# Performance work log

Measured on AMD Instinct MI355X. Metric: run time of the kernel, lower is better.

Reference implementation:

```python
import jax, jax.numpy as jnp
import numpy as np

N_EMB = 1024
N_HEAD = 16
HEAD_DIM = N_EMB // N_HEAD


def setup_inputs() -> dict:
    key = jax.random.key(0)
    k_x, k_wa, k_ba, k_wp, k_bp = jax.random.split(key, 5)
    B, S = 4, 2048
    scale = 1.0 / np.sqrt(N_EMB)
    return {
        "x": jax.random.normal(k_x, (B, S, N_EMB), dtype=jnp.float32),
        "W_attn": jax.random.normal(k_wa, (N_EMB, 3 * N_EMB), dtype=jnp.float32) * scale,
        "b_attn": jax.random.normal(k_ba, (3 * N_EMB,), dtype=jnp.float32) * 0.01,
        "W_proj": jax.random.normal(k_wp, (N_EMB, N_EMB), dtype=jnp.float32) * scale,
        "b_proj": jax.random.normal(k_bp, (N_EMB,), dtype=jnp.float32) * 0.01,
    }


def _attention(x, W_attn, b_attn, W_proj, b_proj):
    B, S, E = x.shape
    qkv = x @ W_attn + b_attn  # [B, S, 3E]
    q, k, v = jnp.split(qkv, 3, axis=-1)
    # [B, H, S, D]
    q = q.reshape(B, S, N_HEAD, HEAD_DIM).transpose(0, 2, 1, 3)
    k = k.reshape(B, S, N_HEAD, HEAD_DIM).transpose(0, 2, 1, 3)
    v = v.reshape(B, S, N_HEAD, HEAD_DIM).transpose(0, 2, 1, 3)
    scores = jnp.einsum("bhqd,bhkd->bhqk", q, k) / jnp.sqrt(jnp.asarray(HEAD_DIM, x.dtype))
    causal = jnp.tril(jnp.ones((S, S), dtype=bool))
    scores = jnp.where(causal, scores, jnp.asarray(-jnp.inf, x.dtype))
    probs = jax.nn.softmax(scores, axis=-1)
    y = jnp.einsum("bhqk,bhkd->bhqd", probs, v)  # [B, H, S, D]
    y = y.transpose(0, 2, 1, 3).reshape(B, S, E)
    return y @ W_proj + b_proj


def reference(x, W_attn, b_attn, W_proj, b_proj):
    return _attention(x, W_attn, b_attn, W_proj, b_proj)
```

## Files before the change

### kernel.cpp

```cpp
#include <hip/hip_runtime.h>
#include <hip/hip_bf16.h>

typedef __bf16 bf16x8 __attribute__((ext_vector_type(8)));
typedef __bf16 bf16x4 __attribute__((ext_vector_type(4)));
typedef float f32x4 __attribute__((ext_vector_type(4)));

#define MFMA16(a, b, c) __builtin_amdgcn_mfma_f32_16x16x32_bf16(a, b, c, 0, 0, 0)

#define BATCH 4
#define SEQ   2048
#define EMB   1024
#define NHEAD 16
#define HDIM  64
#define ROWS  (BATCH * SEQ)
#define N_QKV (3 * EMB)
#define BH_STRIDE (SEQ * HDIM)

__device__ __forceinline__ void gload_lds16(const __bf16* gp, __bf16* lp) {
  __builtin_amdgcn_global_load_lds(
      (const __attribute__((address_space(1))) void*)gp,
      (__attribute__((address_space(3))) void*)lp, 16, 0, 0);
}

__global__ void cast_f32_to_bf16_x4(const float* __restrict__ src,
                                    __bf16* __restrict__ dst, int n4) {
  int i = blockIdx.x * blockDim.x + threadIdx.x;
  if (i >= n4) return;
  float4 f = ((const float4*)src)[i];
  bf16x4 o;
  o.x = (__bf16)f.x; o.y = (__bf16)f.y; o.z = (__bf16)f.z; o.w = (__bf16)f.w;
  ((bf16x4*)dst)[i] = o;
}

__global__ void transpose_to_bf16(const float* __restrict__ src,
                                  __bf16* __restrict__ dst, int R, int C) {
  __shared__ float t[32][33];
  int c0 = blockIdx.x * 32, r0 = blockIdx.y * 32;
  int tx = threadIdx.x, ty = threadIdx.y;
#pragma unroll
  for (int i = 0; i < 32; i += 8)
    t[ty + i][tx] = src[(size_t)(r0 + ty + i) * C + c0 + tx];
  __syncthreads();
#pragma unroll
  for (int i = 0; i < 32; i += 8)
    dst[(size_t)(c0 + ty + i) * R + r0 + tx] = (__bf16)t[tx][ty + i];
}

__global__ __launch_bounds__(256) void gemm_qkv(
    const __bf16* __restrict__ A, const __bf16* __restrict__ Bt,
    const float* __restrict__ bias,
    __bf16* __restrict__ Qt, __bf16* __restrict__ Kt, __bf16* __restrict__ Vt) {
  const int K = EMB;
  __shared__ __align__(16) __bf16 sA[128 * 32];
  __shared__ __align__(16) __bf16 sB[128 * 32];
  int id = blockIdx.x;
  int xcd = id & 7, j5 = id >> 3;
  int by = j5 >> 3;
  int bx = xcd * 8 + (j5 & 7);
  int m0 = by * 128, n0 = bx * 128;
  int tid = threadIdx.x;
  int wave = tid >> 6, lane = tid & 63;
  int wr = wave >> 1, wc = wave & 1;
  int l16 = lane & 15, quad = lane >> 4, quad4 = quad * 4;
  int f1 = tid * 8;
  int r1 = f1 >> 5, c1 = f1 & 31;
  int f2 = f1 + 2048;
  int r2 = f2 >> 5, c2 = f2 & 31;
  f32x4 acc[4][4] = {};
  for (int k0 = 0; k0 < K; k0 += 32) {
    gload_lds16(A + (size_t)(m0 + r1) * K + k0 + c1, &sA[wave * 512]);
    gload_lds16(A + (size_t)(m0 + r2) * K + k0 + c2, &sA[2048 + wave * 512]);
    gload_lds16(Bt + (size_t)(n0 + r1) * K + k0 + c1, &sB[wave * 512]);
    gload_lds16(Bt + (size_t)(n0 + r2) * K + k0 + c2, &sB[2048 + wave * 512]);
    __syncthreads();
    bf16x8 a[4], b[4];
#pragma unroll
    for (int i = 0; i < 4; i++)
      a[i] = *(const bf16x8*)(sA + (wr * 64 + i * 16 + l16) * 32 + quad * 8);
#pragma unroll
    for (int j = 0; j < 4; j++)
      b[j] = *(const bf16x8*)(sB + (wc * 64 + j * 16 + l16) * 32 + quad * 8);
#pragma unroll
    for (int i = 0; i < 4; i++)
#pragma unroll
      for (int j = 0; j < 4; j++) acc[i][j] = MFMA16(a[i], b[j], acc[i][j]);
    __syncthreads();
  }
  const float KSC = 0.18033688011112043f;
  int sec = m0 >> 10;
#pragma unroll
  for (int i = 0; i < 4; i++) {
    int e0 = m0 + wr * 64 + i * 16 + quad4;
    float4 bv4 = *(const float4*)(bias + e0);
    int h = (e0 & 1023) >> 6, d0 = e0 & 63;
#pragma unroll
    for (int j = 0; j < 4; j++) {
      int scol = n0 + wc * 64 + j * 16 + l16;
      int bidx = scol >> 11, s = scol & 2047;
      size_t base = (size_t)(bidx * NHEAD + h) * BH_STRIDE;
      float v0 = acc[i][j][0] + bv4.x;
      float v1 = acc[i][j][1] + bv4.y;
      float v2 = acc[i][j][2] + bv4.z;
      float v3 = acc[i][j][3] + bv4.w;
      if (sec == 0) {
        int idx = (s >> 4) * 1024 + (d0 >> 5) * 512 + ((d0 >> 3) & 3) * 128 +
                  (s & 15) * 8 + (d0 & 7);
        bf16x4 o4;
        o4.x = (__bf16)(v0 * KSC); o4.y = (__bf16)(v1 * KSC);
        o4.z = (__bf16)(v2 * KSC); o4.w = (__bf16)(v3 * KSC);
        *(bf16x4*)(Qt + base + idx) = o4;
      } else if (sec == 1) {
        int idx = (s >> 6) * 4096 + ((s >> 4) & 3) * 1024 + (d0 >> 5) * 512 +
                  ((d0 >> 3) & 3) * 128 + (s & 15) * 8 + (d0 & 7);
        bf16x4 o4;
        o4.x = (__bf16)v0; o4.y = (__bf16)v1;
        o4.z = (__bf16)v2; o4.w = (__bf16)v3;
        *(bf16x4*)(Kt + base + idx) = o4;
      } else {
        int idx = (s >> 6) * 4096 + (d0 >> 4) * 1024 + ((s >> 5) & 1) * 512 +
                  ((s >> 3) & 3) * 128 + (s & 7) + quad4 * 8;
        Vt[base + idx] = (__bf16)v0;
        Vt[base + idx + 8] = (__bf16)v1;
        Vt[base + idx + 16] = (__bf16)v2;
        Vt[base + idx + 24] = (__bf16)v3;
      }
    }
  }
}

#define PS2 68
__global__ __launch_bounds__(256, 3) void attn_fwd(
    const __bf16* __restrict__ Qt, const __bf16* __restrict__ Kt,
    const __bf16* __restrict__ Vt, __bf16* __restrict__ Y) {
  __shared__ __align__(16) __bf16 sK[2][4096];
  __shared__ __align__(16) __bf16 sV[2][4096];
  __shared__ __align__(16) __bf16 pbuf[4][32 * PS2];
  int id = blockIdx.x;
  int g = id >> 6;
  int qb = 15 - g;
  int hb = id & 63;
  int h = hb >> 2, b = hb & 3;
  int tid = threadIdx.x;
  int wave = tid >> 6, lane = tid & 63;
  int l16 = lane & 15, quad = lane >> 4, quad4 = quad * 4;
  int q0 = qb * 128;
  size_t bh = (size_t)b * NHEAD + h;
  const __bf16* Qh = Qt + bh * BH_STRIDE;
  const __bf16* Kh = Kt + bh * BH_STRIDE;
  const __bf16* Vh = Vt + bh * BH_STRIDE;
  int mq = q0 + wave * 32;
  const __bf16* qbase = Qh + (size_t)(mq >> 4) * 1024 + lane * 8;
  bf16x8 qa0 = *(const bf16x8*)(qbase);
  bf16x8 qa1 = *(const bf16x8*)(qbase + 512);
  bf16x8 qb0 = *(const bf16x8*)(qbase + 1024);
  bf16x8 qb1 = *(const bf16x8*)(qbase + 1536);
  f32x4 accA[4] = {}, accB[4] = {};
  float lA = 0.f, lB = 0.f;
  const float NEG_INF = -__builtin_inff();
  __bf16* pwA = pbuf[wave];
  __bf16* pwB = pbuf[wave] + 16 * PS2;
  int nt = (q0 + 128) >> 6;
  gload_lds16(Kh + tid * 8, sK[0] + tid * 8);
  gload_lds16(Kh + 2048 + tid * 8, sK[0] + 2048 + tid * 8);
  gload_lds16(Vh + tid * 8, sV[0] + tid * 8);
  gload_lds16(Vh + 2048 + tid * 8, sV[0] + 2048 + tid * 8);
  __syncthreads();
  int cur = 0;
  for (int it = 0; it < nt; ++it) {
    int kt = it * 64;
    if (it + 1 < nt) {
      const __bf16* kg = Kh + (size_t)(it + 1) * 4096 + tid * 8;
      const __bf16* vg = Vh + (size_t)(it + 1) * 4096 + tid * 8;
      __bf16* dK = sK[cur ^ 1] + tid * 8;
      __bf16* dV = sV[cur ^ 1] + tid * 8;
      gload_lds16(kg, dK);
      gload_lds16(kg + 2048, dK + 2048);
      gload_lds16(vg, dV);
      gload_lds16(vg + 2048, dV + 2048);
    }
    const __bf16* sKc = sK[cur];
    const __bf16* sVc = sV[cur];
    bool diag = (kt + 64 > mq);
    int relA = mq + l16 - kt;
#pragma unroll
    for (int t = 0; t < 4; t++) {
      bf16x8 ka = *(const bf16x8*)(sKc + t * 1024 + lane * 8);
      bf16x8 kb = *(const bf16x8*)(sKc + t * 1024 + 512 + lane * 8);
      f32x4 zA = {}, zB = {};
      zA = MFMA16(ka, qa0, zA);
      zA = MFMA16(kb, qa1, zA);
      zB = MFMA16(ka, qb0, zB);
      zB = MFMA16(kb, qb1, zB);
      int kl = t * 16 + quad4;
      float pA[4], pB[4];
      if (diag) {
        int relB = relA + 16;
#pragma unroll
        for (int r = 0; r < 4; r++) {
          pA[r] = __builtin_amdgcn_exp2f(kl + r > relA ? NEG_INF : zA[r]);
          pB[r] = __builtin_amdgcn_exp2f(kl + r > relB ? NEG_INF : zB[r]);
        }
      } else {
#pragma unroll
        for (int r = 0; r < 4; r++) {
          pA[r] = __builtin_amdgcn_exp2f(zA[r]);
          pB[r] = __builtin_amdgcn_exp2f(zB[r]);
        }
      }
      lA += (pA[0] + pA[1]) + (pA[2] + pA[3]);
      lB += (pB[0] + pB[1]) + (pB[2] + pB[3]);
      bf16x4 oA, oB;
      oA.x = (__bf16)pA[0]; oA.y = (__bf16)pA[1];
      oA.z = (__bf16)pA[2]; oA.w = (__bf16)pA[3];
      oB.x = (__bf16)pB[0]; oB.y = (__bf16)pB[1];
      oB.z = (__bf16)pB[2]; oB.w = (__bf16)pB[3];
      *(bf16x4*)(pwA + l16 * PS2 + kl) = oA;
      *(bf16x4*)(pwB + l16 * PS2 + kl) = oB;
    }
    bf16x8 pA0 = *(const bf16x8*)(pwA + l16 * PS2 + quad * 8);
    bf16x8 pA1 = *(const bf16x8*)(pwA + l16 * PS2 + 32 + quad * 8);
    bf16x8 pB0 = *(const bf16x8*)(pwB + l16 * PS2 + quad * 8);
    bf16x8 pB1 = *(const bf16x8*)(pwB + l16 * PS2 + 32 + quad * 8);
#pragma unroll
    for (int jj = 0; jj < 4; jj++) {
      bf16x8 va = *(const bf16x8*)(sVc + jj * 1024 + lane * 8);
      bf16x8 vb = *(const bf16x8*)(sVc + jj * 1024 + 512 + lane * 8);
      accA[jj] = MFMA16(va, pA0, accA[jj]);
      accA[jj] = MFMA16(vb, pA1, accA[jj]);
      accB[jj] = MFMA16(va, pB0, accB[jj]);
      accB[jj] = MFMA16(vb, pB1, accB[jj]);
    }
    __syncthreads();
    cur ^= 1;
  }
  lA += __shfl_xor(lA, 16); lA += __shfl_xor(lA, 32);
  lB += __shfl_xor(lB, 16); lB += __shfl_xor(lB, 32);
  float invA = 1.f / lA, invB = 1.f / lB;
  int gqA = mq + l16, gqB = mq + 16 + l16;
#pragma unroll
  for (int jj = 0; jj < 4; jj++) {
    bf16x4 oA, oB;
    oA.x = (__bf16)(accA[jj][0] * invA);
    oA.y = (__bf16)(accA[jj][1] * invA);
    oA.z = (__bf16)(accA[jj][2] * invA);
    oA.w = (__bf16)(accA[jj][3] * invA);
    oB.x = (__bf16)(accB[jj][0] * invB);
    oB.y = (__bf16)(accB[jj][1] * invB);
    oB.z = (__bf16)(accB[jj][2] * invB);
    oB.w = (__bf16)(accB[jj][3] * invB);
    *(bf16x4*)(Y + ((size_t)b * SEQ + gqA) * EMB + h * HDIM + jj * 16 + quad4) = oA;
    *(bf16x4*)(Y + ((size_t)b * SEQ + gqB) * EMB + h * HDIM + jj * 16 + quad4) = oB;
  }
}

__global__ __launch_bounds__(256) void gemm_proj(
    const __bf16* __restrict__ A, const __bf16* __restrict__ Bt,
    const float* __restrict__ bias, float* __restrict__ out) {
  const int K = EMB;
  __shared__ __align__(16) __bf16 sA[128 * 32];
  __shared__ __align__(16) __bf16 sB[128 * 32];
  int id = blockIdx.x;
  int lid = (id & 7) * (512 >> 3) + (id >> 3);
  int bx = lid & 7, by = lid >> 3;
  int m0 = by * 128, n0 = bx * 128;
  int tid = threadIdx.x;
  int wave = tid >> 6, lane = tid & 63;
  int wr = wave >> 1, wc = wave & 1;
  int l16 = lane & 15, quad = lane >> 4;
  int f1 = tid * 8;
  int r1 = f1 >> 5, c1 = f1 & 31;
  int f2 = f1 + 2048;
  int r2 = f2 >> 5, c2 = f2 & 31;
  f32x4 acc[4][4] = {};
  for (int k0 = 0; k0 < K; k0 += 32) {
    gload_lds16(A + (size_t)(m0 + r1) * K + k0 + c1, &sA[wave * 512]);
    gload_lds16(A + (size_t)(m0 + r2) * K + k0 + c2, &sA[2048 + wave * 512]);
    gload_lds16(Bt + (size_t)(n0 + r1) * K + k0 + c1, &sB[wave * 512]);
    gload_lds16(Bt + (size_t)(n0 + r2) * K + k0 + c2, &sB[2048 + wave * 512]);
    __syncthreads();
    bf16x8 a[4], b[4];
#pragma unroll
    for (int i = 0; i < 4; i++)
      a[i] = *(const bf16x8*)(sA + (wr * 64 + i * 16 + l16) * 32 + quad * 8);
#pragma unroll
    for (int j = 0; j < 4; j++)
      b[j] = *(const bf16x8*)(sB + (wc * 64 + j * 16 + l16) * 32 + quad * 8);
#pragma unroll
    for (int i = 0; i < 4; i++)
#pragma unroll
      for (int j = 0; j < 4; j++) acc[i][j] = MFMA16(a[i], b[j], acc[i][j]);
    __syncthreads();
  }
#pragma unroll
  for (int i = 0; i < 4; i++) {
    int row = m0 + wr * 64 + i * 16 + quad * 4;
#pragma unroll
    for (int j = 0; j < 4; j++) {
      int col = n0 + wc * 64 + j * 16 + l16;
      float bv = bias[col];
#pragma unroll
      for (int r = 0; r < 4; r++)
        out[(size_t)(row + r) * EMB + col] = acc[i][j][r] + bv;
    }
  }
}

extern "C" void kernel_launch(void* const* d_in, const int* in_sizes, int n_in,
                              void* d_out, int out_size, void* d_ws, size_t ws_size,
                              hipStream_t stream) {
  const float* x      = (const float*)d_in[0];
  const float* W_attn = (const float*)d_in[1];
  const float* b_attn = (const float*)d_in[2];
  const float* W_proj = (const float*)d_in[3];
  const float* b_proj = (const float*)d_in[4];
  float* out = (float*)d_out;

  char* ws = (char*)d_ws;
  size_t off = 0;
  __bf16* xb   = (__bf16*)(ws + off); off += (size_t)ROWS * EMB * 2;
  __bf16* Wa_t = (__bf16*)(ws + off); off += (size_t)N_QKV * EMB * 2;
  __bf16* Wp_t = (__bf16*)(ws + off); off += (size_t)EMB * EMB * 2;
  __bf16* Qt   = (__bf16*)(ws + off); off += (size_t)ROWS * EMB * 2;
  __bf16* Kt   = (__bf16*)(ws + off); off += (size_t)ROWS * EMB * 2;
  __bf16* Vt   = (__bf16*)(ws + off); off += (size_t)ROWS * EMB * 2;
  __bf16* Yb   = (__bf16*)(ws + off); off += (size_t)ROWS * EMB * 2;

  {
    int n4 = ROWS * EMB / 4;
    cast_f32_to_bf16_x4<<<(n4 + 255) / 256, 256, 0, stream>>>(x, xb, n4);
    dim3 blk(32, 8);
    transpose_to_bf16<<<dim3(N_QKV / 32, EMB / 32), blk, 0, stream>>>(W_attn, Wa_t, EMB, N_QKV);
    transpose_to_bf16<<<dim3(EMB / 32, EMB / 32), blk, 0, stream>>>(W_proj, Wp_t, EMB, EMB);
  }
  gemm_qkv<<<dim3(1536), 256, 0, stream>>>(Wa_t, xb, b_attn, Qt, Kt, Vt);
  attn_fwd<<<dim3((SEQ / 128) * NHEAD * BATCH), 256, 0, stream>>>(Qt, Kt, Vt, Yb);
  gemm_proj<<<dim3(512), 256, 0, stream>>>(Yb, Wp_t, b_proj, out);
}
```

Measured before the change: 253.6 us.

## Keep softmax probabilities in registers by permuting V layout, skip masked tiles

The V tensor layout written by the QKV projection is permuted so the MFMA output fragment of the score tile can be fed directly as the B operand of the PV MFMA. This removes the per-wave LDS round trip for probabilities, along with its buffer and the extra LDS traffic. The change also skips compute for key tiles that lie fully above the causal diagonal for a wave, raises wave priority around the MFMA section, and increases the launch-bounds occupancy hint from 3 to 4 blocks. Correctness depends on the new V index mapping exactly matching the register k-ordering, and the higher occupancy hint may force register spills.

```diff
diff --git a/kernel.cpp b/kernel.cpp
--- a/kernel.cpp
+++ b/kernel.cpp
@@ -118,7 +118,8 @@
         *(bf16x4*)(Kt + base + idx) = o4;
       } else {
         int idx = (s >> 6) * 4096 + (d0 >> 4) * 1024 + ((s >> 5) & 1) * 512 +
-                  ((s >> 3) & 3) * 128 + (s & 7) + quad4 * 8;
+                  ((s >> 2) & 3) * 128 + ((s >> 4) & 1) * 4 + (s & 3) +
+                  quad4 * 8;
         Vt[base + idx] = (__bf16)v0;
         Vt[base + idx + 8] = (__bf16)v1;
         Vt[base + idx + 16] = (__bf16)v2;
@@ -128,13 +129,11 @@
   }
 }
 
-#define PS2 68
-__global__ __launch_bounds__(256, 3) void attn_fwd(
+__global__ __launch_bounds__(256, 4) void attn_fwd(
     const __bf16* __restrict__ Qt, const __bf16* __restrict__ Kt,
     const __bf16* __restrict__ Vt, __bf16* __restrict__ Y) {
   __shared__ __align__(16) __bf16 sK[2][4096];
   __shared__ __align__(16) __bf16 sV[2][4096];
-  __shared__ __align__(16) __bf16 pbuf[4][32 * PS2];
   int id = blockIdx.x;
   int g = id >> 6;
   int qb = 15 - g;
@@ -157,8 +156,6 @@
   f32x4 accA[4] = {}, accB[4] = {};
   float lA = 0.f, lB = 0.f;
   const float NEG_INF = -__builtin_inff();
-  __bf16* pwA = pbuf[wave];
-  __bf16* pwB = pbuf[wave] + 16 * PS2;
   int nt = (q0 + 128) >> 6;
   gload_lds16(Kh + tid * 8, sK[0] + tid * 8);
   gload_lds16(Kh + 2048 + tid * 8, sK[0] + 2048 + tid * 8);
@@ -178,57 +175,72 @@
       gload_lds16(vg, dV);
       gload_lds16(vg + 2048, dV + 2048);
     }
-    const __bf16* sKc = sK[cur];
-    const __bf16* sVc = sV[cur];
-    bool diag = (kt + 64 > mq);
-    int relA = mq + l16 - kt;
-#pragma unroll
-    for (int t = 0; t < 4; t++) {
-      bf16x8 ka = *(const bf16x8*)(sKc + t * 1024 + lane * 8);
-      bf16x8 kb = *(const bf16x8*)(sKc + t * 1024 + 512 + lane * 8);
-      f32x4 zA = {}, zB = {};
-      zA = MFMA16(ka, qa0, zA);
-      zA = MFMA16(kb, qa1, zA);
-      zB = MFMA16(ka, qb0, zB);
-      zB = MFMA16(kb, qb1, zB);
-      int kl = t * 16 + quad4;
-      float pA[4], pB[4];
-      if (diag) {
-        int relB = relA + 16;
-#pragma unroll
-        for (int r = 0; r < 4; r++) {
-          pA[r] = __builtin_amdgcn_exp2f(kl + r > relA ? NEG_INF : zA[r]);
-          pB[r] = __builtin_amdgcn_exp2f(kl + r > relB ? NEG_INF : zB[r]);
+    if (kt <= mq + 31) {
+      const __bf16* sKc = sK[cur];
+      const __bf16* sVc = sV[cur];
+      bool diag = (kt + 64 > mq);
+      int relA = mq + l16 - kt;
+      int relB = relA + 16;
+      bf16x8 PA0, PA1, PB0, PB1;
+      __builtin_amdgcn_s_setprio(1);
+#pragma unroll
+      for (int t = 0; t < 4; t++) {
+        bf16x8 ka = *(const bf16x8*)(sKc + t * 1024 + lane * 8);
+        bf16x8 kb = *(const bf16x8*)(sKc + t * 1024 + 512 + lane * 8);
+        f32x4 zA = {}, zB = {};
+        zA = MFMA16(ka, qa0, zA);
+        zA = MFMA16(kb, qa1, zA);
+        zB = MFMA16(ka, qb0, zB);
+        zB = MFMA16(kb, qb1, zB);
+        int kl = t * 16 + quad4;
+        float pA[4], pB[4];
+        if (diag) {
+#pragma unroll
+          for (int r = 0; r < 4; r++) {
+            pA[r] = __builtin_amdgcn_exp2f(kl + r > relA ? NEG_INF : zA[r]);
+            pB[r] = __builtin_amdgcn_exp2f(kl + r > relB ? NEG_INF : zB[r]);
+          }
+        } else {
+#pragma unroll
+          for (int r = 0; r < 4; r++) {
+            pA[r] = __builtin_amdgcn_exp2f(zA[r]);
+            pB[r] = __builtin_amdgcn_exp2f(zB[r]);
+          }
         }
-      } else {
-#pragma unroll
-        for (int r = 0; r < 4; r++) {
-          pA[r] = __builtin_amdgcn_exp2f(zA[r]);
-          pB[r] = __builtin_amdgcn_exp2f(zB[r]);
+        lA += (pA[0] + pA[1]) + (pA[2] + pA[3]);
+        lB += (pB[0] + pB[1]) + (pB[2] + pB[3]);
+        if (t == 0) {
+          PA0[0] = (__bf16)pA[0]; PA0[1] = (__bf16)pA[1];
+          PA0[2] = (__bf16)pA[2]; PA0[3] = (__bf16)pA[3];
+          PB0[0] = (__bf16)pB[0]; PB0[1] = (__bf16)pB[1];
+          PB0[2] = (__bf16)pB[2]; PB0[3] = (__bf16)pB[3];
+        } else if (t == 1) {
+          PA0[4] = (__bf16)pA[0]; PA0[5] = (__bf16)pA[1];
+          PA0[6] = (__bf16)pA[2]; PA0[7] = (__bf16)pA[3];
+          PB0[4] = (__bf16)pB[0]; PB0[5] = (__bf16)pB[1];
+          PB0[6] = (__bf16)pB[2]; PB0[7] = (__bf16)pB[3];
+        } else if (t == 2) {
+          PA1[0] = (__bf16)pA[0]; PA1[1] = (__bf16)pA[1];
+          PA1[2] = (__bf16)pA[2]; PA1[3] = (__bf16)pA[3];
+          PB1[0] = (__bf16)pB[0]; PB1[1] = (__bf16)pB[1];
+          PB1[2] = (__bf16)pB[2]; PB1[3] = (__bf16)pB[3];
+        } else {
+          PA1[4] = (__bf16)pA[0]; PA1[5] = (__bf16)pA[1];
+          PA1[6] = (__bf16)pA[2]; PA1[7] = (__bf16)pA[3];
+          PB1[4] = (__bf16)pB[0]; PB1[5] = (__bf16)pB[1];
+          PB1[6] = (__bf16)pB[2]; PB1[7] = (__bf16)pB[3];
         }
       }
-      lA += (pA[0] + pA[1]) + (pA[2] + pA[3]);
-      lB += (pB[0] + pB[1]) + (pB[2] + pB[3]);
-      bf16x4 oA, oB;
-      oA.x = (__bf16)pA[0]; oA.y = (__bf16)pA[1];
-      oA.z = (__bf16)pA[2]; oA.w = (__bf16)pA[3];
-      oB.x = (__bf16)pB[0]; oB.y = (__bf16)pB[1];
-      oB.z = (__bf16)pB[2]; oB.w = (__bf16)pB[3];
-      *(bf16x4*)(pwA + l16 * PS2 + kl) = oA;
-      *(bf16x4*)(pwB + l16 * PS2 + kl) = oB;
-    }
-    bf16x8 pA0 = *(const bf16x8*)(pwA + l16 * PS2 + quad * 8);
-    bf16x8 pA1 = *(const bf16x8*)(pwA + l16 * PS2 + 32 + quad * 8);
-    bf16x8 pB0 = *(const bf16x8*)(pwB + l16 * PS2 + quad * 8);
-    bf16x8 pB1 = *(const bf16x8*)(pwB + l16 * PS2 + 32 + quad * 8);
-#pragma unroll
-    for (int jj = 0; jj < 4; jj++) {
-      bf16x8 va = *(const bf16x8*)(sVc + jj * 1024 + lane * 8);
-      bf16x8 vb = *(const bf16x8*)(sVc + jj * 1024 + 512 + lane * 8);
-      accA[jj] = MFMA16(va, pA0, accA[jj]);
-      accA[jj] = MFMA16(vb, pA1, accA[jj]);
-      accB[jj] = MFMA16(va, pB0, accB[jj]);
-      accB[jj] = MFMA16(vb, pB1, accB[jj]);
+#pragma unroll
+      for (int jj = 0; jj < 4; jj++) {
+        bf16x8 va = *(const bf16x8*)(sVc + jj * 1024 + lane * 8);
+        bf16x8 vb = *(const bf16x8*)(sVc + jj * 1024 + 512 + lane * 8);
+        accA[jj] = MFMA16(va, PA0, accA[jj]);
+        accA[jj] = MFMA16(vb, PA1, accA[jj]);
+        accB[jj] = MFMA16(va, PB0, accB[jj]);
+        accB[jj] = MFMA16(vb, PB1, accB[jj]);
+      }
+      __builtin_amdgcn_s_setprio(0);
     }
     __syncthreads();
     cur ^= 1;
```

New measurement: 240.8 us. 1.05x faster.
